# Kernel tuning notes

Hardware: AMD Instinct MI355X
Metric: run time of the kernel (lower is better)

## Reference

```python
import jax, jax.numpy as jnp
import numpy as np

B, S, H, NH = 8, 1024, 768, 12
DK = H // NH  # 64


def setup_inputs() -> dict:
    key = jax.random.key(0)
    ks = jax.random.split(key, 7)
    sc = 0.02
    return {
        "Q": jax.random.normal(ks[0], (B, S, H), jnp.float32),
        "K": jax.random.normal(ks[1], (B, S, H), jnp.float32),
        "V": jax.random.normal(ks[2], (B, S, H), jnp.float32),
        "Wq": jax.random.normal(ks[3], (H, H), jnp.float32) * sc,
        "Wk": jax.random.normal(ks[4], (H, H), jnp.float32) * sc,
        "Wv": jax.random.normal(ks[5], (H, H), jnp.float32) * sc,
        "Wo": jax.random.normal(ks[6], (H, H), jnp.float32) * sc,
    }


def reference(Q, K, V, Wq, Wk, Wv, Wo):
    # torch Linear(bias=False): y = x @ W.T, weight shape [out, in]
    q = jnp.einsum('bsh,oh->bso', Q, Wq).reshape(B, S, NH, DK)
    k = jnp.einsum('bsh,oh->bso', K, Wk).reshape(B, S, NH, DK)
    v = jnp.einsum('bsh,oh->bso', V, Wv).reshape(B, S, NH, DK)
    # naive SDPA per head: full [B,NH,S,S] score matrix, scale by sqrt(dk)
    scores = jnp.einsum('bqnd,bknd->bnqk', q, k) / jnp.sqrt(jnp.float32(DK))
    w = jax.nn.softmax(scores, axis=-1)
    c = jnp.einsum('bnqk,bknd->bqnd', w, v).reshape(B, S, H)
    return jnp.einsum('bsh,oh->bso', c, Wo)
```

## Files before the change

### kernel.cpp

```cpp
#include <hip/hip_runtime.h>
#include <hip/hip_bf16.h>

#define B_   8
#define S_   1024
#define H_   768
#define NH_  12
#define DK_  64
#define M_   (B_ * S_)

typedef __attribute__((ext_vector_type(8))) short          short8;
typedef __attribute__((ext_vector_type(8))) unsigned short ushort8;
typedef __attribute__((ext_vector_type(4))) unsigned short ushort4v;
typedef __attribute__((ext_vector_type(4))) float          f32x4;

__device__ __forceinline__ unsigned short f2bf(float x) {
    union { __hip_bfloat16 h; unsigned short u; } r;
    r.h = __float2bfloat16(x);
    return r.u;
}

__device__ __forceinline__ unsigned cvtpk_bf16(float lo, float hi) {
    unsigned r;
    asm("v_cvt_pk_bf16_f32 %0, %1, %2" : "=v"(r) : "v"(lo), "v"(hi));
    return r;
}

__global__ __launch_bounds__(256)
void cvt_w(const float* __restrict__ w0, const float* __restrict__ w1,
           const float* __restrict__ w2, const float* __restrict__ w3,
           unsigned short* __restrict__ o0, unsigned short* __restrict__ o1,
           unsigned short* __restrict__ o2, unsigned short* __restrict__ o3)
{
    const int wsel = blockIdx.y;
    const float* src = (wsel == 0) ? w0 : (wsel == 1) ? w1 : (wsel == 2) ? w2 : w3;
    unsigned short* dst = (wsel == 0) ? o0 : (wsel == 1) ? o1 : (wsel == 2) ? o2 : o3;
    const float s = (wsel == 0) ? 0.125f * 1.44269504089f : 1.0f;
    const int i = blockIdx.x * 256 + threadIdx.x;
    const float4 x = ((const float4*)src)[i];
    ushort4v o;
    o[0] = f2bf(x.x * s); o[1] = f2bf(x.y * s);
    o[2] = f2bf(x.z * s); o[3] = f2bf(x.w * s);
    ((ushort4v*)dst)[i] = o;
}

template<bool A_BF16, bool OUT_BF16>
__global__ __launch_bounds__(256)
void gemm_bt(const void* __restrict__ A0, const void* __restrict__ A1,
             const void* __restrict__ A2,
             const unsigned short* __restrict__ W0,
             const unsigned short* __restrict__ W1,
             const unsigned short* __restrict__ W2,
             void* __restrict__ C0, void* __restrict__ C1, void* __restrict__ C2)
{
    __shared__ unsigned short As[128 * 32];
    __shared__ unsigned short Bs[128 * 32];

    const int tid  = threadIdx.x;
    const int z    = blockIdx.z;
    const int bm   = blockIdx.x, bn = blockIdx.y;
    const int w    = tid >> 6, lane = tid & 63;
    const int lg   = lane >> 4, lc = lane & 15;
    const int wm   = (w >> 1) * 64, wn = (w & 1) * 64;

    const void* Av = (z == 0) ? A0 : (z == 1) ? A1 : A2;
    const unsigned short* Bw = (z == 0) ? W0 : (z == 1) ? W1 : W2;
    void* Cv = (z == 0) ? C0 : (z == 1) ? C1 : C2;

    const float*          Af = (const float*)Av;
    const unsigned short* Ah = (const unsigned short*)Av;

    f32x4 acc[4][4] = {};

    for (int k0 = 0; k0 < H_; k0 += 32) {
        if (A_BF16) {
#pragma unroll
            for (int i = 0; i < 2; i++) {
                const int gI = i * 256 + tid;
                const int row = gI >> 2, c8 = (gI & 3) * 8;
                *(ushort8*)&As[row * 32 + c8] =
                    *(const ushort8*)&Ah[(size_t)(bm * 128 + row) * H_ + k0 + c8];
            }
        } else {
#pragma unroll
            for (int i = 0; i < 4; i++) {
                const int gI = i * 256 + tid;
                const int row = gI >> 3, c4 = (gI & 7) * 4;
                const float4 x = *(const float4*)&Af[(size_t)(bm * 128 + row) * H_ + k0 + c4];
                ushort4v o4;
                o4[0] = f2bf(x.x); o4[1] = f2bf(x.y);
                o4[2] = f2bf(x.z); o4[3] = f2bf(x.w);
                *(ushort4v*)&As[row * 32 + c4] = o4;
            }
        }
#pragma unroll
        for (int i = 0; i < 2; i++) {
            const int gI = i * 256 + tid;
            const int row = gI >> 2, c8 = (gI & 3) * 8;
            *(ushort8*)&Bs[row * 32 + c8] =
                *(const ushort8*)&Bw[(size_t)(bn * 128 + row) * H_ + k0 + c8];
        }
        __syncthreads();

        short8 af[4], bfr[4];
#pragma unroll
        for (int mi = 0; mi < 4; mi++)
            af[mi] = *(const short8*)&As[(wm + mi * 16 + lc) * 32 + lg * 8];
#pragma unroll
        for (int ni = 0; ni < 4; ni++)
            bfr[ni] = *(const short8*)&Bs[(wn + ni * 16 + lc) * 32 + lg * 8];
#pragma unroll
        for (int mi = 0; mi < 4; mi++)
#pragma unroll
            for (int ni = 0; ni < 4; ni++)
                acc[mi][ni] = __builtin_amdgcn_mfma_f32_16x16x32_bf16(
                    af[mi], bfr[ni], acc[mi][ni], 0, 0, 0);
        __syncthreads();
    }

#pragma unroll
    for (int mi = 0; mi < 4; mi++)
#pragma unroll
        for (int ni = 0; ni < 4; ni++)
#pragma unroll
            for (int reg = 0; reg < 4; reg++) {
                const int row = bm * 128 + wm + mi * 16 + lg * 4 + reg;
                const int col = bn * 128 + wn + ni * 16 + lc;
                if (OUT_BF16)
                    ((unsigned short*)Cv)[(size_t)row * H_ + col] = f2bf(acc[mi][ni][reg]);
                else
                    ((float*)Cv)[(size_t)row * H_ + col] = acc[mi][ni][reg];
            }
}

__global__ __launch_bounds__(256)
void transpose_v(const unsigned short* __restrict__ v,
                 unsigned short* __restrict__ vt)
{
    __shared__ unsigned short T[64][72];
    const int tid = threadIdx.x;
    const int st0 = blockIdx.x, h = blockIdx.y, b = blockIdx.z;
    const int r = tid >> 2, d0 = (tid & 3) * 16, g = tid & 3;

    const unsigned short* src = &v[(size_t)(b * S_ + st0 * 64 + r) * H_ + h * DK_ + d0];
    const ushort8 v0 = *(const ushort8*)src;
    const ushort8 v1 = *(const ushort8*)(src + 8);
    const int colv = r ^ (g << 4);
#pragma unroll
    for (int j = 0; j < 8; j++) T[d0 + j][colv]     = v0[j];
#pragma unroll
    for (int j = 0; j < 8; j++) T[d0 + 8 + j][colv] = v1[j];
    __syncthreads();

    const size_t ob = ((size_t)(b * NH_ + h) * DK_) * S_ + st0 * 64;
#pragma unroll
    for (int half = 0; half < 2; half++) {
        const int ci = half * 256 + tid;
        const int d = ci >> 3, kc = ci & 7;
        const int sw = ((d >> 4) & 3) << 4;
        const ushort8 val = *(const ushort8*)&T[d][(kc * 8) ^ sw];
        *(ushort8*)&vt[ob + (size_t)d * S_ + kc * 8] = val;
    }
}

__global__ __launch_bounds__(256)
void attn(const unsigned short* __restrict__ q,
          const unsigned short* __restrict__ k,
          const unsigned short* __restrict__ vt,
          unsigned short* __restrict__ c)
{
    __shared__ unsigned short Ks[64][72];
    __shared__ unsigned short Vs[64][72];

    const int tid  = threadIdx.x;
    const int qt   = blockIdx.x, h = blockIdx.y, b = blockIdx.z;
    const int wid  = tid >> 6;
    const int lane = tid & 63;
    const int lg   = lane >> 4, lc = lane & 15;
    const int r    = tid >> 2;
    const int g    = tid & 3;
    const int d0   = g * 16;
    const size_t base = (size_t)b * S_ * H_ + (size_t)h * DK_;
    const size_t vtb  = (size_t)(b * NH_ + h) * DK_ * S_;

    short8 aq[2][2];
#pragma unroll
    for (int m = 0; m < 2; m++)
#pragma unroll
        for (int ks = 0; ks < 2; ks++)
            aq[m][ks] = *(const short8*)
                &q[base + (size_t)(qt * 128 + wid * 32 + m * 16 + lc) * H_ + ks * 32 + lg * 8];

    f32x4 o[2][4] = {};
    float lsum[2] = {0.f, 0.f};

    for (int kt = 0; kt < S_ / 64; kt++) {
        {
            const unsigned short* ksrc = &k[base + (size_t)(kt * 64 + r) * H_ + d0];
            *(ushort8*)&Ks[r][d0]     = *(const ushort8*)ksrc;
            *(ushort8*)&Ks[r][d0 + 8] = *(const ushort8*)(ksrc + 8);
            const unsigned short* vsrc = &vt[vtb + (size_t)r * S_ + kt * 64 + d0];
            *(ushort8*)&Vs[r][d0]     = *(const ushort8*)vsrc;
            *(ushort8*)&Vs[r][d0 + 8] = *(const ushort8*)(vsrc + 8);
        }
        __syncthreads();

        f32x4 st[2][4] = {};
        __builtin_amdgcn_s_setprio(1);
#pragma unroll
        for (int ni = 0; ni < 4; ni++)
#pragma unroll
            for (int ks = 0; ks < 2; ks++) {
                const short8 bk = *(const short8*)&Ks[ni * 16 + lc][ks * 32 + lg * 8];
                st[0][ni] = __builtin_amdgcn_mfma_f32_16x16x32_bf16(bk, aq[0][ks], st[0][ni], 0, 0, 0);
                st[1][ni] = __builtin_amdgcn_mfma_f32_16x16x32_bf16(bk, aq[1][ks], st[1][ni], 0, 0, 0);
            }
        __builtin_amdgcn_s_setprio(0);

        unsigned pw[2][4][2];
#pragma unroll
        for (int m = 0; m < 2; m++) {
#pragma unroll
            for (int ni = 0; ni < 4; ni++) {
#pragma unroll
                for (int reg = 0; reg < 4; reg++) {
                    const float pp = exp2f(st[m][ni][reg]);
                    st[m][ni][reg] = pp;
                    lsum[m] += pp;
                }
                pw[m][ni][0] = cvtpk_bf16(st[m][ni][0], st[m][ni][1]);
                pw[m][ni][1] = cvtpk_bf16(st[m][ni][2], st[m][ni][3]);
            }
        }

        const int sl0 = lc + ((lg & 1) << 5);
        const int sl1 = sl0 + 16;
        const bool hi = (lg >> 1) != 0;
        short8 pa[2][2];
#pragma unroll
        for (int m = 0; m < 2; m++)
#pragma unroll
            for (int ks = 0; ks < 2; ks++) {
                const unsigned lo0 = pw[m][2 * ks][0],     lo1 = pw[m][2 * ks][1];
                const unsigned hi0 = pw[m][2 * ks + 1][0], hi1 = pw[m][2 * ks + 1][1];
                union { unsigned u[4]; short8 s8; } pk;
                const unsigned a0l = __shfl(lo0, sl0, 64), a0h = __shfl(hi0, sl0, 64);
                const unsigned a1l = __shfl(lo1, sl0, 64), a1h = __shfl(hi1, sl0, 64);
                const unsigned a2l = __shfl(lo0, sl1, 64), a2h = __shfl(hi0, sl1, 64);
                const unsigned a3l = __shfl(lo1, sl1, 64), a3h = __shfl(hi1, sl1, 64);
                pk.u[0] = hi ? a0h : a0l;
                pk.u[1] = hi ? a1h : a1l;
                pk.u[2] = hi ? a2h : a2l;
                pk.u[3] = hi ? a3h : a3l;
                pa[m][ks] = pk.s8;
            }

        __builtin_amdgcn_s_setprio(1);
#pragma unroll
        for (int ni = 0; ni < 4; ni++)
#pragma unroll
            for (int ks = 0; ks < 2; ks++) {
                const short8 bv = *(const short8*)&Vs[ni * 16 + lc][ks * 32 + lg * 8];
                o[0][ni] = __builtin_amdgcn_mfma_f32_16x16x32_bf16(pa[0][ks], bv, o[0][ni], 0, 0, 0);
                o[1][ni] = __builtin_amdgcn_mfma_f32_16x16x32_bf16(pa[1][ks], bv, o[1][ni], 0, 0, 0);
            }
        __builtin_amdgcn_s_setprio(0);
        __syncthreads();
    }

#pragma unroll
    for (int m = 0; m < 2; m++) {
        float l = lsum[m];
        l += __shfl_xor(l, 16, 64);
        l += __shfl_xor(l, 32, 64);
        const float iv = 1.0f / l;
#pragma unroll
        for (int reg = 0; reg < 4; reg++) {
            const float ivr = __shfl(iv, lg * 4 + reg, 64);
            const int row = qt * 128 + wid * 32 + m * 16 + lg * 4 + reg;
#pragma unroll
            for (int ni = 0; ni < 4; ni++)
                c[base + (size_t)row * H_ + ni * 16 + lc] = f2bf(o[m][ni][reg] * ivr);
        }
    }
}

extern "C" void kernel_launch(void* const* d_in, const int* in_sizes, int n_in,
                              void* d_out, int out_size, void* d_ws, size_t ws_size,
                              hipStream_t stream)
{
    const float* Q  = (const float*)d_in[0];
    const float* K  = (const float*)d_in[1];
    const float* V  = (const float*)d_in[2];
    const float* Wq = (const float*)d_in[3];
    const float* Wk = (const float*)d_in[4];
    const float* Wv = (const float*)d_in[5];
    const float* Wo = (const float*)d_in[6];

    unsigned short* qb = (unsigned short*)d_ws;
    unsigned short* kb = qb + (size_t)M_ * H_;
    unsigned short* vb = kb + (size_t)M_ * H_;
    unsigned short* vtb = vb + (size_t)M_ * H_;
    unsigned short* cb  = vb;
    unsigned short* wq = vtb + (size_t)M_ * H_;
    unsigned short* wk = wq + (size_t)H_ * H_;
    unsigned short* wv = wk + (size_t)H_ * H_;
    unsigned short* wo = wv + (size_t)H_ * H_;

    cvt_w<<<dim3(H_ * H_ / 4 / 256, 4), 256, 0, stream>>>(
        Wq, Wk, Wv, Wo, wq, wk, wv, wo);

    gemm_bt<false, true><<<dim3(M_ / 128, H_ / 128, 3), 256, 0, stream>>>(
        Q, K, V, wq, wk, wv, qb, kb, vb);

    transpose_v<<<dim3(S_ / 64, NH_, B_), 256, 0, stream>>>(vb, vtb);

    attn<<<dim3(S_ / 128, NH_, B_), 256, 0, stream>>>(qb, kb, vtb, cb);

    gemm_bt<true, false><<<dim3(M_ / 128, H_ / 128, 1), 256, 0, stream>>>(
        cb, cb, cb, wo, wo, wo, d_out, d_out, d_out);
}
```

Before: 156.7 us.

## Use direct global-to-LDS loads and XCD-aware block remapping in projection GEMMs

Replaces the register-staged bf16 tile loads in the projection GEMM with global_load_lds direct-to-LDS transfers for the weight tile and the bf16 activation tile, and rewrites the fp32 activation staging to 8-element chunks. Also flattens the grid to 1D and remaps block ids so consecutive blocks on the same XCD (bid&7) share M rows and weight tiles, aiming at better L2 reuse. This cuts VGPR traffic and load instructions but relies on the LDS layout produced by per-wave 16-byte direct loads matching the original row-major tile layout.

```diff
diff --git a/kernel.cpp b/kernel.cpp
--- a/kernel.cpp
+++ b/kernel.cpp
@@ -23,6 +23,12 @@
     unsigned r;
     asm("v_cvt_pk_bf16_f32 %0, %1, %2" : "=v"(r) : "v"(lo), "v"(hi));
     return r;
+}
+
+__device__ __forceinline__ void glds16(const unsigned short* g, unsigned short* l) {
+    __builtin_amdgcn_global_load_lds(
+        (const __attribute__((address_space(1))) unsigned int*)g,
+        (__attribute__((address_space(3))) unsigned int*)l, 16, 0, 0);
 }
 
 __global__ __launch_bounds__(256)
@@ -56,8 +62,13 @@
     __shared__ unsigned short Bs[128 * 32];
 
     const int tid  = threadIdx.x;
-    const int z    = blockIdx.z;
-    const int bm   = blockIdx.x, bn = blockIdx.y;
+    const int bid  = blockIdx.x;
+    const int x    = bid & 7, j = bid >> 3;
+    const int z    = j / 48;
+    const int r48  = j % 48;
+    const int bm   = x * 8 + r48 / 6;
+    const int bn   = r48 % 6;
+
     const int w    = tid >> 6, lane = tid & 63;
     const int lg   = lane >> 4, lc = lane & 15;
     const int wm   = (w >> 1) * 64, wn = (w & 1) * 64;
@@ -69,35 +80,38 @@
     const float*          Af = (const float*)Av;
     const unsigned short* Ah = (const unsigned short*)Av;
 
+    const int srow = tid >> 2;
+    const int sc8  = (tid & 3) * 8;
+
+    const unsigned short* gB  = &Bw[(size_t)(bn * 128 + srow) * H_ + sc8];
+    unsigned short* ldsB0 = &Bs[w * 512];
+    unsigned short* ldsB1 = &Bs[2048 + w * 512];
+
+    const unsigned short* gAh = A_BF16 ? &Ah[(size_t)(bm * 128 + srow) * H_ + sc8] : nullptr;
+    const float*          gAf = A_BF16 ? nullptr : &Af[(size_t)(bm * 128 + srow) * H_ + sc8];
+    unsigned short* ldsA0 = &As[w * 512];
+    unsigned short* ldsA1 = &As[2048 + w * 512];
+
     f32x4 acc[4][4] = {};
 
     for (int k0 = 0; k0 < H_; k0 += 32) {
+        glds16(gB + k0, ldsB0);
+        glds16(gB + (size_t)64 * H_ + k0, ldsB1);
         if (A_BF16) {
+            glds16(gAh + k0, ldsA0);
+            glds16(gAh + (size_t)64 * H_ + k0, ldsA1);
+        } else {
 #pragma unroll
             for (int i = 0; i < 2; i++) {
-                const int gI = i * 256 + tid;
-                const int row = gI >> 2, c8 = (gI & 3) * 8;
-                *(ushort8*)&As[row * 32 + c8] =
-                    *(const ushort8*)&Ah[(size_t)(bm * 128 + row) * H_ + k0 + c8];
-            }
-        } else {
-#pragma unroll
-            for (int i = 0; i < 4; i++) {
-                const int gI = i * 256 + tid;
-                const int row = gI >> 3, c4 = (gI & 7) * 4;
-                const float4 x = *(const float4*)&Af[(size_t)(bm * 128 + row) * H_ + k0 + c4];
-                ushort4v o4;
-                o4[0] = f2bf(x.x); o4[1] = f2bf(x.y);
-                o4[2] = f2bf(x.z); o4[3] = f2bf(x.w);
-                *(ushort4v*)&As[row * 32 + c4] = o4;
-            }
-        }
-#pragma unroll
-        for (int i = 0; i < 2; i++) {
-            const int gI = i * 256 + tid;
-            const int row = gI >> 2, c8 = (gI & 3) * 8;
-            *(ushort8*)&Bs[row * 32 + c8] =
-                *(const ushort8*)&Bw[(size_t)(bn * 128 + row) * H_ + k0 + c8];
+                const float4 x0 = *(const float4*)(gAf + (size_t)i * 64 * H_ + k0);
+                const float4 x1 = *(const float4*)(gAf + (size_t)i * 64 * H_ + k0 + 4);
+                ushort8 o8;
+                o8[0] = f2bf(x0.x); o8[1] = f2bf(x0.y);
+                o8[2] = f2bf(x0.z); o8[3] = f2bf(x0.w);
+                o8[4] = f2bf(x1.x); o8[5] = f2bf(x1.y);
+                o8[6] = f2bf(x1.z); o8[7] = f2bf(x1.w);
+                *(ushort8*)&As[(i * 64 + srow) * 32 + sc8] = o8;
+            }
         }
         __syncthreads();
 
@@ -309,13 +323,13 @@
     cvt_w<<<dim3(H_ * H_ / 4 / 256, 4), 256, 0, stream>>>(
         Wq, Wk, Wv, Wo, wq, wk, wv, wo);
 
-    gemm_bt<false, true><<<dim3(M_ / 128, H_ / 128, 3), 256, 0, stream>>>(
+    gemm_bt<false, true><<<dim3(64 * 6 * 3), 256, 0, stream>>>(
         Q, K, V, wq, wk, wv, qb, kb, vb);
 
     transpose_v<<<dim3(S_ / 64, NH_, B_), 256, 0, stream>>>(vb, vtb);
 
     attn<<<dim3(S_ / 128, NH_, B_), 256, 0, stream>>>(qb, kb, vtb, cb);
 
-    gemm_bt<true, false><<<dim3(M_ / 128, H_ / 128, 1), 256, 0, stream>>>(
+    gemm_bt<true, false><<<dim3(64 * 6), 256, 0, stream>>>(
         cb, cb, cb, wo, wo, wo, d_out, d_out, d_out);
 }
```

Measured after the change: 157.7 us. About the same (+0.6%).
